# Kernel tuning notes

Hardware: AMD Instinct MI355X
Metric: run time of the kernel (lower is better)

Reference implementation:

```python
import jax, jax.numpy as jnp
import numpy as np
from jax import lax

COCO_80_TO_91 = [1,2,3,4,5,6,7,8,9,10,11,13,14,15,16,17,18,19,20,21,22,23,24,25,27,28,31,32,33,34,35,36,37,38,39,40,41,42,43,44,46,47,48,49,50,51,52,53,54,55,56,57,58,59,60,61,62,63,64,65,67,70,72,73,74,75,76,77,78,79,80,81,82,84,85,86,87,88,89,90]

CONF = 0.25      # self.confidence
IOU_THR = 0.7    # ultralytics NMS default
TOPK = 1000      # candidate cap before NMS
MAX_DET = 300    # ultralytics max_det default
MAX_WH = 7680.0  # per-class offset trick
IMG_SZ = 640.0   # yolov8 letterboxed input size


def setup_inputs() -> dict:
    key = jax.random.key(0)
    preds = jax.random.uniform(key, (32, 84, 8400), dtype=jnp.float32)
    return {"preds": preds}


def _nms_single(boxes, scores):
    """Greedy NMS on score-descending boxes [K,4] (class-offset xyxy). Returns keep mask [K]."""
    K = boxes.shape[0]
    area = (boxes[:, 2] - boxes[:, 0]) * (boxes[:, 3] - boxes[:, 1])  # [K]
    lt = jnp.maximum(boxes[:, None, :2], boxes[None, :, :2])          # [K,K,2]
    rb = jnp.minimum(boxes[:, None, 2:], boxes[None, :, 2:])
    wh = jnp.clip(rb - lt, 0.0)
    inter = wh[..., 0] * wh[..., 1]
    iou = inter / (area[:, None] + area[None, :] - inter + 1e-7)       # [K,K]
    idx = jnp.arange(K)
    sup = (iou > IOU_THR) & (idx[None, :] > idx[:, None])              # i suppresses later j

    def body(i, keep):
        return jnp.where(keep[i], keep & ~sup[i], keep)

    return lax.fori_loop(0, K, body, jnp.ones((K,), dtype=bool))


def reference(preds):
    # preds: [B, 84, N] -> [B, N, 84]
    p = jnp.transpose(preds, (0, 2, 1))
    box_xywh = p[..., :4] * IMG_SZ           # xywh in pixels on 640x640 canvas
    cls = p[..., 4:]                          # [B, N, 80]
    scores = jnp.max(cls, axis=-1)            # best-class confidence
    labels = jnp.argmax(cls, axis=-1)         # 0..79
    xy, wh = box_xywh[..., :2], box_xywh[..., 2:]
    xyxy = jnp.concatenate([xy - wh * 0.5, xy + wh * 0.5], axis=-1)  # decode

    # confidence filter + top-K candidate selection (score-descending)
    s_masked = jnp.where(scores > CONF, scores, -1.0)
    top_s, top_i = lax.top_k(s_masked, TOPK)                          # [B,TOPK]
    top_b = jnp.take_along_axis(xyxy, top_i[..., None], axis=1)      # [B,TOPK,4]
    top_l = jnp.take_along_axis(labels, top_i, axis=1)               # [B,TOPK]

    # per-class NMS via class offset
    off_b = top_b + (top_l.astype(top_b.dtype) * MAX_WH)[..., None]
    keep = jax.vmap(_nms_single)(off_b, top_s) & (top_s > CONF)

    # select final max_det detections, zero-pad invalid slots
    fin_s = jnp.where(keep, top_s, -1.0)
    out_s, out_i = lax.top_k(fin_s, MAX_DET)                          # [B,MAX_DET]
    out_b = jnp.take_along_axis(top_b, out_i[..., None], axis=1)
    out_l = jnp.take_along_axis(top_l, out_i, axis=1)
    valid = out_s > CONF
    boxes = jnp.where(valid[..., None], out_b, 0.0)
    scores_out = jnp.where(valid, out_s, 0.0)
    mapped = jnp.asarray(COCO_80_TO_91, dtype=jnp.int64)[out_l]       # COCO 80 -> 91 ids
    labels_out = jnp.where(valid, mapped, 0)
    return boxes, scores_out, labels_out
```

## Files before the change

kernel.cpp:

```cpp
#include <hip/hip_runtime.h>
#include <stdint.h>

typedef unsigned long long u64;
typedef unsigned int u32;

#define BATCH 32
#define NCH 84
#define NA 8400
#define NCLS 80
#define TOPK 1000
#define MAXDET 300
#define CONF 0.25f
#define IOU_T 0.7f
#define MAX_WH 7680.0f
#define IMG_SZ 640.0f
#define NT 1024
#define KPT 9
#define NCOPY 8
#define HPAD 260

__device__ __constant__ float coco_map_f[NCLS] = {
    1,2,3,4,5,6,7,8,9,10,11,13,14,15,16,17,18,19,20,21,22,23,24,25,27,28,
    31,32,33,34,35,36,37,38,39,40,41,42,43,44,46,47,48,49,50,51,52,53,54,
    55,56,57,58,59,60,61,62,63,64,65,67,70,72,73,74,75,76,77,78,79,80,81,
    82,84,85,86,87,88,89,90};

__device__ inline u64 shflx64(u64 v, int m) {
    int lo = __shfl_xor((int)(u32)(v & 0xFFFFFFFFull), m, 64);
    int hi = __shfl_xor((int)(u32)(v >> 32), m, 64);
    return ((u64)(u32)hi << 32) | (u32)lo;
}

__global__ __launch_bounds__(256)
void decode_kernel(const float* __restrict__ preds,
                   u64* __restrict__ keys,
                   float4* __restrict__ boxes) {
    const int b = blockIdx.y;
    const int a = blockIdx.x * 256 + threadIdx.x;
    const bool live = (a < NA);
    const int ac = live ? a : (NA - 1);
    const float* p = preds + (size_t)b * NCH * NA + ac;

    float bx = p[0];
    float by = p[(size_t)1 * NA];
    float bw = p[(size_t)2 * NA];
    float bh = p[(size_t)3 * NA];

    const float* pc = p + (size_t)4 * NA;
    float best = -1.0f;
    int bl = 0;
#pragma unroll 16
    for (int r = 0; r < NCLS; ++r) {
        float v = pc[(size_t)r * NA];
        bl = (v > best) ? r : bl;
        best = fmaxf(v, best);
    }

    if (live) {
        float fx = bx * IMG_SZ, fy = by * IMG_SZ;
        float fw = bw * IMG_SZ, fh = bh * IMG_SZ;
        float hw = fw * 0.5f, hh = fh * 0.5f;
        boxes[(size_t)b * NA + a] = make_float4(fx - hw, fy - hh, fx + hw, fy + hh);
        float s = (best > CONF) ? best : -1.0f;
        u32 fb = __float_as_uint(s);
        u32 u = (fb & 0x80000000u) ? ~fb : (fb | 0x80000000u);
        keys[(size_t)b * NA + a] =
            ((u64)u << 21) | ((u64)(16383 - a) << 7) | (u64)bl;
    }
}

__global__ __launch_bounds__(NT, 4)
void select_sort_kernel(const u64* __restrict__ keys,
                        u64* __restrict__ sortedk) {
    const int b = blockIdx.x;
    const int t = threadIdx.x;
    const int lane = t & 63, wid = t >> 6;

    __shared__ struct {
        u64 sk[2][NT];
        int hist[NCOPY * HPAD];
    } u_s;
    __shared__ int selB, selK, hselS, cnt_s;
    __shared__ int wsum[16], woff[16];

    u64 kreg[KPT];
    const u64* kb = keys + (size_t)b * NA;
#pragma unroll
    for (int j = 0; j < KPT; ++j) {
        int i = t + j * NT;
        kreg[j] = (i < NA) ? kb[i] : 0ull;
    }

    u64 P = 0ull;
    int kk = TOPK;
    int nsel = 0;
    bool done = false;
    bool did16 = false;

    {
        int dg[KPT];
        int mymax = -1;
#pragma unroll
        for (int j = 0; j < KPT; ++j) {
            dg[j] = (kreg[j] != 0ull) ? (int)((kreg[j] >> 37) & 0xFFFF) : -1;
            mymax = max(mymax, dg[j]);
        }
#pragma unroll
        for (int off = 32; off; off >>= 1)
            mymax = max(mymax, __shfl_down(mymax, off, 64));
        if (lane == 0) wsum[wid] = mymax;
        __syncthreads();
        int maxd = wsum[0];
#pragma unroll
        for (int q = 1; q < 16; ++q) maxd = max(maxd, wsum[q]);
        int myc = 0;
#pragma unroll
        for (int j = 0; j < KPT; ++j) myc += (dg[j] == maxd) ? 1 : 0;
#pragma unroll
        for (int off = 32; off; off >>= 1) myc += __shfl_down(myc, off, 64);
        if (lane == 0) woff[wid] = myc;
        __syncthreads();
        int cm = 0;
#pragma unroll
        for (int q = 0; q < 16; ++q) cm += woff[q];
        if (cm >= kk) {
            P = ((u64)maxd) << 37;
            nsel = cm;
            did16 = true;
            done = (nsel <= NT);
        }
    }

    if (!done) {
        const int dstart = did16 ? 1 : 3;
        for (int d = dstart; d >= 0; --d) {
            const int sh = 21 + 8 * d;
            const u64 hmask = (~0ull) << (sh + 8);
            int dig[KPT];
            int mymax = -1;
#pragma unroll
            for (int j = 0; j < KPT; ++j) {
                bool act = (((kreg[j] ^ P) & hmask) == 0ull) && (kreg[j] != 0ull);
                dig[j] = act ? (int)((kreg[j] >> sh) & 255) : -1;
                mymax = max(mymax, dig[j]);
            }
#pragma unroll
            for (int off = 32; off; off >>= 1)
                mymax = max(mymax, __shfl_down(mymax, off, 64));
            if (lane == 0) wsum[wid] = mymax;
            __syncthreads();
            int maxb = wsum[0];
#pragma unroll
            for (int q = 1; q < 16; ++q) maxb = max(maxb, wsum[q]);
            int myc = 0;
#pragma unroll
            for (int j = 0; j < KPT; ++j) myc += (dig[j] == maxb) ? 1 : 0;
#pragma unroll
            for (int off = 32; off; off >>= 1) myc += __shfl_down(myc, off, 64);
            if (lane == 0) woff[wid] = myc;
            __syncthreads();
            int cm = 0;
#pragma unroll
            for (int q = 0; q < 16; ++q) cm += woff[q];
            if (cm >= kk) {
                P |= ((u64)maxb) << sh;
                nsel = TOPK - kk + cm;
                if (nsel <= NT) break;
                continue;
            }
            for (int i = t; i < NCOPY * HPAD; i += NT) u_s.hist[i] = 0;
            __syncthreads();
            int* myh = u_s.hist + (wid & (NCOPY - 1)) * HPAD;
#pragma unroll
            for (int j = 0; j < KPT; ++j)
                if (dig[j] >= 0) atomicAdd(&myh[dig[j]], 1);
            __syncthreads();
            if (t < 64) {
                int h0 = 0, h1 = 0, h2 = 0, h3 = 0;
                for (int c = 0; c < NCOPY; ++c) {
                    const int* hp = u_s.hist + c * HPAD + 4 * t;
                    h0 += hp[0]; h1 += hp[1]; h2 += hp[2]; h3 += hp[3];
                }
                int s = h0 + h1 + h2 + h3;
                int S = s;
                #pragma unroll
                for (int off = 1; off < 64; off <<= 1) {
                    int o = __shfl_down(S, off, 64);
                    if (t + off < 64) S += o;
                }
                int Snext = S - s;
                int c3 = Snext + h3, c2 = c3 + h2, c1 = c2 + h1, c0 = c1 + h0;
                int cand = -1, above = 0;
                if (c0 >= kk) {
                    if      (c3 >= kk) { cand = 4 * t + 3; above = Snext; }
                    else if (c2 >= kk) { cand = 4 * t + 2; above = c3; }
                    else if (c1 >= kk) { cand = 4 * t + 1; above = c2; }
                    else               { cand = 4 * t;     above = c1; }
                }
                int pc = (cand < 0) ? 0 : (((cand + 1) << 16) | (kk - above));
                #pragma unroll
                for (int off = 32; off; off >>= 1)
                    pc = max(pc, __shfl_down(pc, off, 64));
                pc = __shfl(pc, 0, 64);
                int B = (pc >> 16) - 1;
                if (t == (B >> 2)) {
                    int m4 = B & 3;
                    selB = B;
                    selK = pc & 0xFFFF;
                    hselS = (m4 == 0) ? h0 : (m4 == 1) ? h1 : (m4 == 2) ? h2 : h3;
                }
            }
            __syncthreads();
            P |= ((u64)selB) << sh;
            kk = selK;
            nsel = TOPK - kk + hselS;
            if (nsel <= NT) break;
        }
    }

    __syncthreads();
    if (t == 0) cnt_s = 0;
    __syncthreads();
#pragma unroll
    for (int j = 0; j < KPT; ++j) {
        bool p = (kreg[j] >= P);
        u64 m = __ballot(p);
        int base = 0;
        if (lane == 0) base = atomicAdd(&cnt_s, (int)__popcll(m));
        base = __shfl(base, 0, 64);
        if (p) {
            int pos = base + (int)__popcll(m & ((1ull << lane) - 1ull));
            if (pos < NT) u_s.sk[0][pos] = kreg[j];
        }
    }
    if (t < NT - nsel) u_s.sk[0][nsel + t] = 0ull;
    __syncthreads();

    u64 myk = u_s.sk[0][t];
    int buf = 1;
    for (int size = 2; size <= NT; size <<= 1) {
        bool up = ((t & size) == 0);
        for (int stride = size >> 1; stride; stride >>= 1) {
            u64 pk;
            if (stride >= 64) {
                u_s.sk[buf][t] = myk;
                __syncthreads();
                pk = u_s.sk[buf][t ^ stride];
                buf ^= 1;
            } else {
                pk = shflx64(myk, stride);
            }
            bool tlow = ((t & stride) == 0);
            u64 mn = (myk < pk) ? myk : pk;
            u64 mx = (myk < pk) ? pk : myk;
            myk = up ? (tlow ? mx : mn) : (tlow ? mn : mx);
        }
    }
    sortedk[(size_t)b * NT + t] = myk;
}

__global__ __launch_bounds__(64)
void nms_kernel(const u64* __restrict__ sortedk,
                const float4* __restrict__ boxes,
                unsigned char* __restrict__ keepg) {
    const int c = blockIdx.x;
    const int b = blockIdx.y;
    const int lane = threadIdx.x;
    const u64* skb = sortedk + (size_t)b * NT;

    __shared__ int idxs[64];

    int total = 0;
#pragma unroll
    for (int i = 0; i < 16; ++i) {
        int pos = i * 64 + lane;
        u64 k = skb[pos];
        bool match = (pos < TOPK) && ((int)(k & 127ull) == c);
        u64 m = __ballot(match);
        if (match) {
            int r = total + (int)__popcll(m & ((1ull << lane) - 1ull));
            if (r < 64) idxs[r] = pos;
        }
        total += (int)__popcll(m);
    }
    __syncthreads();
    const int n = total;
    if (n == 0) return;

    if (n <= 64) {
        float4 bb = make_float4(0.f, 0.f, 0.f, 0.f);
        float ar = 0.f;
        int rk = 0;
        if (lane < n) {
            rk = idxs[lane];
            u64 k = skb[rk];
            int anc = 16383 - (int)((k >> 7) & 16383ull);
            float4 g = boxes[(size_t)b * NA + anc];
            float off = (float)c * MAX_WH;
            bb = make_float4(g.x + off, g.y + off, g.z + off, g.w + off);
            ar = (bb.z - bb.x) * (bb.w - bb.y);
        }
        u64 colm = 0ull;
        for (int i = 0; i < n; ++i) {
            float hx0 = __shfl(bb.x, i, 64);
            float hy0 = __shfl(bb.y, i, 64);
            float hx1 = __shfl(bb.z, i, 64);
            float hy1 = __shfl(bb.w, i, 64);
            float ha  = __shfl(ar, i, 64);
            float lx = fmaxf(hx0, bb.x), ly = fmaxf(hy0, bb.y);
            float rx = fminf(hx1, bb.z), ry = fminf(hy1, bb.w);
            float w = fmaxf(rx - lx, 0.0f);
            float h = fmaxf(ry - ly, 0.0f);
            float inter = w * h;
            float denom = ha + ar;
            denom = denom - inter;
            denom = denom + 1e-7f;
            bool s = (lane > i) && (lane < n) && (inter / denom > IOU_T);
            colm |= ((u64)s) << i;
        }
        u64 alive = (n >= 64) ? ~0ull : ((1ull << n) - 1ull);
        for (int i = 0; i < n; ++i) {
            if (!((alive >> i) & 1ull)) continue;
            alive &= ~__ballot((colm >> i) & 1ull);
        }
        if (lane < n) keepg[(size_t)b * NT + rk] = (unsigned char)((alive >> lane) & 1ull);
    } else if (lane == 0) {
        const float off = (float)c * MAX_WH;
        u64 aliveW[16];
        for (int q = 0; q < 16; ++q) aliveW[q] = ~0ull;
        for (int i = 0; i < TOPK; ++i) {
            if ((int)(skb[i] & 127ull) != c) continue;
            if (!((aliveW[i >> 6] >> (i & 63)) & 1ull)) continue;
            int anci = 16383 - (int)((skb[i] >> 7) & 16383ull);
            float4 g = boxes[(size_t)b * NA + anci];
            float ix0 = g.x + off, iy0 = g.y + off;
            float ix1 = g.z + off, iy1 = g.w + off;
            float ai = (ix1 - ix0) * (iy1 - iy0);
            for (int jj = i + 1; jj < TOPK; ++jj) {
                if ((int)(skb[jj] & 127ull) != c) continue;
                if (!((aliveW[jj >> 6] >> (jj & 63)) & 1ull)) continue;
                int ancj = 16383 - (int)((skb[jj] >> 7) & 16383ull);
                float4 h = boxes[(size_t)b * NA + ancj];
                float jx0 = h.x + off, jy0 = h.y + off;
                float jx1 = h.z + off, jy1 = h.w + off;
                float aj = (jx1 - jx0) * (jy1 - jy0);
                float lx = fmaxf(ix0, jx0), ly = fmaxf(iy0, jy0);
                float rx = fminf(ix1, jx1), ry = fminf(iy1, jy1);
                float ww = fmaxf(rx - lx, 0.0f);
                float hh = fmaxf(ry - ly, 0.0f);
                float inter = ww * hh;
                float denom = ai + aj;
                denom = denom - inter;
                denom = denom + 1e-7f;
                if (inter / denom > IOU_T) aliveW[jj >> 6] &= ~(1ull << (jj & 63));
            }
        }
        for (int i = 0; i < TOPK; ++i)
            if ((int)(skb[i] & 127ull) == c)
                keepg[(size_t)b * NT + i] = (unsigned char)((aliveW[i >> 6] >> (i & 63)) & 1ull);
    }
}

__global__ __launch_bounds__(NT)
void epilogue_kernel(const u64* __restrict__ sortedk,
                     const unsigned char* __restrict__ keepg,
                     const float4* __restrict__ boxes,
                     float* __restrict__ out) {
    const int b = blockIdx.x;
    const int t = threadIdx.x;
    const int lane = t & 63, wid = t >> 6;
    __shared__ int wsum[16], woff[16], ktot_s;

    u64 myk = sortedk[(size_t)b * NT + t];
    bool valid = false;
    float sj = 0.0f;
    if (t < TOPK) {
        u32 u = (u32)(myk >> 21);
        u32 fb = (u & 0x80000000u) ? (u ^ 0x80000000u) : ~u;
        sj = __uint_as_float(fb);
        valid = keepg[(size_t)b * NT + t] && (sj > CONF);
    }
    u64 m = __ballot(valid);
    if (lane == 0) wsum[wid] = (int)__popcll(m);
    __syncthreads();
    if (wid == 0) {
        int v = (lane < 16) ? wsum[lane] : 0;
        #pragma unroll
        for (int off = 1; off < 16; off <<= 1) {
            int o = __shfl_up(v, off, 64);
            if (lane >= off) v += o;
        }
        if (lane < 16) woff[lane] = v - wsum[lane];
        if (lane == 15) ktot_s = v;
    }
    __syncthreads();
    int ktot = ktot_s;
    int rank = woff[wid] + (int)__popcll(m & ((1ull << lane) - 1ull));

    float* out_boxes = out;
    float* out_scores = out + (size_t)BATCH * MAXDET * 4;
    float* out_labels = out + (size_t)BATCH * MAXDET * 5;
    if (valid && rank < MAXDET) {
        int anc = 16383 - (int)((myk >> 7) & 16383ull);
        float4 bx = boxes[(size_t)b * NA + anc];
        float* ob = out_boxes + ((size_t)b * MAXDET + rank) * 4;
        ob[0] = bx.x; ob[1] = bx.y; ob[2] = bx.z; ob[3] = bx.w;
        out_scores[(size_t)b * MAXDET + rank] = sj;
        out_labels[(size_t)b * MAXDET + rank] = coco_map_f[(int)(myk & 127ull)];
    }
    if (t < MAXDET && t >= ktot) {
        float* ob = out_boxes + ((size_t)b * MAXDET + t) * 4;
        ob[0] = 0.0f; ob[1] = 0.0f; ob[2] = 0.0f; ob[3] = 0.0f;
        out_scores[(size_t)b * MAXDET + t] = 0.0f;
        out_labels[(size_t)b * MAXDET + t] = 0.0f;
    }
}

extern "C" void kernel_launch(void* const* d_in, const int* in_sizes, int n_in,
                              void* d_out, int out_size, void* d_ws, size_t ws_size,
                              hipStream_t stream) {
    const float* preds = (const float*)d_in[0];
    char* ws = (char*)d_ws;
    size_t off = 0;
    auto alloc = [&](size_t bytes) { char* p = ws + off; off += (bytes + 255) & ~(size_t)255; return p; };

    u64* keys            = (u64*)           alloc((size_t)BATCH * NA * 8);
    float4* boxes        = (float4*)        alloc((size_t)BATCH * NA * 16);
    u64* sortedk         = (u64*)           alloc((size_t)BATCH * NT * 8);
    unsigned char* keepg = (unsigned char*) alloc((size_t)BATCH * NT);
    float* out = (float*)d_out;

    dim3 dgrid((NA + 255) / 256, BATCH);
    decode_kernel<<<dgrid, 256, 0, stream>>>(preds, keys, boxes);
    select_sort_kernel<<<BATCH, NT, 0, stream>>>(keys, sortedk);
    dim3 ngrid(NCLS, BATCH);
    nms_kernel<<<ngrid, 64, 0, stream>>>(sortedk, boxes, keepg);
    epilogue_kernel<<<BATCH, NT, 0, stream>>>(sortedk, keepg, boxes, out);
}
```

Measured before the change: 163.3 us.

## Fuse epilogue into NMS kernel via last-block-done atomic counter

Removes the separate epilogue kernel launch by having the last NMS block to finish for each batch image, detected with an atomic counter reset in the decode kernel, perform the compaction and output writes. This saves one kernel launch and its dependency gap. In exchange, the epilogue now runs on a single 64-lane wavefront per image, serially looping over 16 chunks instead of using 1024 threads. It also relies on threadfence ordering for correctness.

After: 215.3 us. 31.9% more time.

```diff
diff --git a/kernel.cpp b/kernel.cpp
--- a/kernel.cpp
+++ b/kernel.cpp
@@ -34,9 +34,11 @@
 __global__ __launch_bounds__(256)
 void decode_kernel(const float* __restrict__ preds,
                    u64* __restrict__ keys,
-                   float4* __restrict__ boxes) {
+                   float4* __restrict__ boxes,
+                   int* __restrict__ done_cnt) {
     const int b = blockIdx.y;
     const int a = blockIdx.x * 256 + threadIdx.x;
+    if (blockIdx.x == 0 && threadIdx.x == 0) done_cnt[b] = 0;
     const bool live = (a < NA);
     const int ac = live ? a : (NA - 1);
     const float* p = preds + (size_t)b * NCH * NA + ac;
@@ -260,9 +262,11 @@
 }
 
 __global__ __launch_bounds__(64)
-void nms_kernel(const u64* __restrict__ sortedk,
-                const float4* __restrict__ boxes,
-                unsigned char* __restrict__ keepg) {
+void nms_epi_kernel(const u64* __restrict__ sortedk,
+                    const float4* __restrict__ boxes,
+                    unsigned char* __restrict__ keepg,
+                    int* __restrict__ done_cnt,
+                    float* __restrict__ out) {
     const int c = blockIdx.x;
     const int b = blockIdx.y;
     const int lane = threadIdx.x;
@@ -285,9 +289,9 @@
     }
     __syncthreads();
     const int n = total;
-    if (n == 0) return;
-
-    if (n <= 64) {
+
+    if (n == 0) {
+    } else if (n <= 64) {
         float4 bb = make_float4(0.f, 0.f, 0.f, 0.f);
         float ar = 0.f;
         int rk = 0;
@@ -359,60 +363,49 @@
             if ((int)(skb[i] & 127ull) == c)
                 keepg[(size_t)b * NT + i] = (unsigned char)((aliveW[i >> 6] >> (i & 63)) & 1ull);
     }
-}
-
-__global__ __launch_bounds__(NT)
-void epilogue_kernel(const u64* __restrict__ sortedk,
-                     const unsigned char* __restrict__ keepg,
-                     const float4* __restrict__ boxes,
-                     float* __restrict__ out) {
-    const int b = blockIdx.x;
-    const int t = threadIdx.x;
-    const int lane = t & 63, wid = t >> 6;
-    __shared__ int wsum[16], woff[16], ktot_s;
-
-    u64 myk = sortedk[(size_t)b * NT + t];
-    bool valid = false;
-    float sj = 0.0f;
-    if (t < TOPK) {
-        u32 u = (u32)(myk >> 21);
-        u32 fb = (u & 0x80000000u) ? (u ^ 0x80000000u) : ~u;
-        sj = __uint_as_float(fb);
-        valid = keepg[(size_t)b * NT + t] && (sj > CONF);
-    }
-    u64 m = __ballot(valid);
-    if (lane == 0) wsum[wid] = (int)__popcll(m);
-    __syncthreads();
-    if (wid == 0) {
-        int v = (lane < 16) ? wsum[lane] : 0;
-        #pragma unroll
-        for (int off = 1; off < 16; off <<= 1) {
-            int o = __shfl_up(v, off, 64);
-            if (lane >= off) v += o;
-        }
-        if (lane < 16) woff[lane] = v - wsum[lane];
-        if (lane == 15) ktot_s = v;
-    }
-    __syncthreads();
-    int ktot = ktot_s;
-    int rank = woff[wid] + (int)__popcll(m & ((1ull << lane) - 1ull));
+
+    __threadfence();
+    int old = 0;
+    if (lane == 0) old = atomicAdd(&done_cnt[b], 1);
+    old = __shfl(old, 0, 64);
+    if (old != NCLS - 1) return;
+    __threadfence();
 
     float* out_boxes = out;
     float* out_scores = out + (size_t)BATCH * MAXDET * 4;
     float* out_labels = out + (size_t)BATCH * MAXDET * 5;
-    if (valid && rank < MAXDET) {
-        int anc = 16383 - (int)((myk >> 7) & 16383ull);
-        float4 bx = boxes[(size_t)b * NA + anc];
-        float* ob = out_boxes + ((size_t)b * MAXDET + rank) * 4;
-        ob[0] = bx.x; ob[1] = bx.y; ob[2] = bx.z; ob[3] = bx.w;
-        out_scores[(size_t)b * MAXDET + rank] = sj;
-        out_labels[(size_t)b * MAXDET + rank] = coco_map_f[(int)(myk & 127ull)];
-    }
-    if (t < MAXDET && t >= ktot) {
-        float* ob = out_boxes + ((size_t)b * MAXDET + t) * 4;
+    const unsigned char* kpb = keepg + (size_t)b * NT;
+
+    int ktot = 0;
+#pragma unroll
+    for (int i = 0; i < 16; ++i) {
+        int pos = i * 64 + lane;
+        u64 k = skb[pos];
+        bool valid = false;
+        float sj = 0.0f;
+        if (pos < TOPK) {
+            u32 u = (u32)(k >> 21);
+            u32 fb = (u & 0x80000000u) ? (u ^ 0x80000000u) : ~u;
+            sj = __uint_as_float(fb);
+            valid = kpb[pos] && (sj > CONF);
+        }
+        u64 m = __ballot(valid);
+        int rank = ktot + (int)__popcll(m & ((1ull << lane) - 1ull));
+        if (valid && rank < MAXDET) {
+            int anc = 16383 - (int)((k >> 7) & 16383ull);
+            float4 bx = boxes[(size_t)b * NA + anc];
+            float* ob = out_boxes + ((size_t)b * MAXDET + rank) * 4;
+            ob[0] = bx.x; ob[1] = bx.y; ob[2] = bx.z; ob[3] = bx.w;
+            out_scores[(size_t)b * MAXDET + rank] = sj;
+            out_labels[(size_t)b * MAXDET + rank] = coco_map_f[(int)(k & 127ull)];
+        }
+        ktot += (int)__popcll(m);
+    }
+    for (int pos = ktot + lane; pos < MAXDET; pos += 64) {
+        float* ob = out_boxes + ((size_t)b * MAXDET + pos) * 4;
         ob[0] = 0.0f; ob[1] = 0.0f; ob[2] = 0.0f; ob[3] = 0.0f;
-        out_scores[(size_t)b * MAXDET + t] = 0.0f;
-        out_labels[(size_t)b * MAXDET + t] = 0.0f;
+        out_scores[(size_t)b * MAXDET + pos] = 0.0f;
+        out_labels[(size_t)b * MAXDET + pos] = 0.0f;
     }
 }
 
@@ -428,12 +421,12 @@
     float4* boxes        = (float4*)        alloc((size_t)BATCH * NA * 16);
     u64* sortedk         = (u64*)           alloc((size_t)BATCH * NT * 8);
     unsigned char* keepg = (unsigned char*) alloc((size_t)BATCH * NT);
+    int* done_cnt        = (int*)           alloc((size_t)BATCH * 4);
     float* out = (float*)d_out;
 
     dim3 dgrid((NA + 255) / 256, BATCH);
-    decode_kernel<<<dgrid, 256, 0, stream>>>(preds, keys, boxes);
+    decode_kernel<<<dgrid, 256, 0, stream>>>(preds, keys, boxes, done_cnt);
     select_sort_kernel<<<BATCH, NT, 0, stream>>>(keys, sortedk);
     dim3 ngrid(NCLS, BATCH);
-    nms_kernel<<<ngrid, 64, 0, stream>>>(sortedk, boxes, keepg);
-    epilogue_kernel<<<BATCH, NT, 0, stream>>>(sortedk, keepg, boxes, out);
+    nms_epi_kernel<<<ngrid, 64, 0, stream>>>(sortedk, boxes, keepg, done_cnt, out);
 }
```
